# Kernel optimization log

Hardware: AMD Instinct MI355X
Metric: run time of the kernel (lower is better)

Reference implementation:

```python
import jax, jax.numpy as jnp
import numpy as np

N_HEADS = 16


def setup_inputs() -> dict:
    key = jax.random.key(0)
    ks = jax.random.split(key, 7)
    B, S, D = 2, 2048, 1024
    x = jax.random.normal(ks[0], (B, S, D), dtype=jnp.float32)
    attn_mask = jax.random.normal(ks[1], (S, S), dtype=jnp.float32) * 0.1
    attn_bias = jax.random.normal(ks[2], (B, S, S), dtype=jnp.float32) * 0.1
    Wqkv = jax.random.normal(ks[3], (D, 3 * D), dtype=jnp.float32) * (D ** -0.5)
    bqkv = jnp.zeros((3 * D,), dtype=jnp.float32)
    Wout = jax.random.normal(ks[4], (D, D), dtype=jnp.float32) * (D ** -0.5)
    bout = jnp.zeros((D,), dtype=jnp.float32)
    return {"x": x, "attn_mask": attn_mask, "attn_bias": attn_bias,
            "Wqkv": Wqkv, "bqkv": bqkv, "Wout": Wout, "bout": bout}


def reference(x, attn_mask, attn_bias, Wqkv, bqkv, Wout, bout):
    B, S, D = x.shape
    H = N_HEADS
    hd = D // H
    # qkv projection: [B,S,3D] -> [3,B,H,S,hd]
    qkv = (x @ Wqkv + bqkv).reshape(B, S, 3, H, hd).transpose(2, 0, 3, 1, 4)
    q, k, v = qkv[0], qkv[1], qkv[2]
    scores = jnp.einsum('bhqd,bhkd->bhqk', q, k) / (hd ** 0.5)
    scores = scores + attn_mask[None, None, :, :] + attn_bias[:, None, :, :]
    attn = jax.nn.softmax(scores, axis=-1)  # dropout p=0.0 (eval)
    out = jnp.einsum('bhqk,bhkd->bhqd', attn, v)
    out = out.transpose(0, 2, 1, 3).reshape(B, S, D)
    return out @ Wout + bout
```

## Files before the change

### kernel.cpp

```cpp
#include <hip/hip_runtime.h>
#include <hip/hip_bf16.h>


#define S_LEN 2048
#define DMODEL 1024
#define NH 16
#define HD 64

typedef __bf16 bf16x8 __attribute__((ext_vector_type(8)));
typedef __bf16 bf16x4 __attribute__((ext_vector_type(4)));
typedef __bf16 bf16x2v __attribute__((ext_vector_type(2)));
typedef float f32x4 __attribute__((ext_vector_type(4)));
typedef short s16x4 __attribute__((ext_vector_type(4)));

#define GLD_LDS16(g, l)                                              \
  __builtin_amdgcn_global_load_lds(                                  \
      (const __attribute__((address_space(1))) unsigned int*)(g),    \
      (__attribute__((address_space(3))) unsigned int*)(l), 16, 0, 0)

#if __has_builtin(__builtin_amdgcn_mfma_f32_16x16x16bf16_1k)
#define HAVE_MFMA_16x16x16_BF16 1
#else
#define HAVE_MFMA_16x16x16_BF16 0
#endif

#if __has_builtin(__builtin_amdgcn_exp2f)
#define EXP2F(x) __builtin_amdgcn_exp2f(x)
#else
static __device__ __forceinline__ float EXP2F(float x) {
  float r;
  asm volatile("v_exp_f32 %0, %1" : "=v"(r) : "v"(x));
  return r;
}
#endif

#define LOG2E 1.44269504f

__global__ __launch_bounds__(256) void preprocess(
    const float* __restrict__ x, const float* __restrict__ mask,
    const float* __restrict__ bias, const float* __restrict__ Wqkv,
    const float* __restrict__ Wout, __bf16* __restrict__ Xb,
    __bf16* __restrict__ Wt, __bf16* __restrict__ Wt2,
    __bf16* __restrict__ MB) {
  __shared__ __align__(16) char smem[64 * 65 * 4];
  const int bid = blockIdx.x;
  const int tid = threadIdx.x;

  if (bid < 4096) {
    int i = bid * 256 + tid;
    float4 v = ((const float4*)x)[i];
    bf16x4 o = {(__bf16)v.x, (__bf16)v.y, (__bf16)v.z, (__bf16)v.w};
    *(bf16x4*)&Xb[(size_t)i * 4] = o;
  } else if (bid < 5120) {
    const float* W;
    __bf16* Wo;
    int ncols, n0, k0;
    if (bid < 4864) {
      int id = bid - 4096;
      W = Wqkv; Wo = Wt; ncols = 3072;
      n0 = (id % 48) * 64; k0 = (id / 48) * 64;
    } else {
      int id = bid - 4864;
      W = Wout; Wo = Wt2; ncols = 1024;
      n0 = (id & 15) * 64; k0 = (id >> 4) * 64;
    }
    float(*tile)[65] = (float(*)[65])smem;
    {
      int c = tid & 63, r4 = tid >> 6;
#pragma unroll
      for (int p = 0; p < 16; ++p) {
        int r = r4 + p * 4;
        tile[r][c] = W[(size_t)(k0 + r) * ncols + n0 + c];
      }
    }
    __syncthreads();
    {
      int cc = (tid & 31) * 2, r8 = tid >> 5;
#pragma unroll
      for (int p = 0; p < 8; ++p) {
        int rr = r8 + p * 8;
        bf16x2v o = {(__bf16)tile[cc][rr], (__bf16)tile[cc + 1][rr]};
        *(bf16x2v*)&Wo[(size_t)(n0 + rr) * 1024 + k0 + cc] = o;
      }
    }
  } else {
    int id = bid - 5120;
    const int kt = id & 31, qt = (id >> 5) & 31, b = id >> 10;
    __bf16(*sm)[68] = (__bf16(*)[68])smem;
    {
      const int r0 = tid >> 4;
      const int cc = (tid & 15) * 4;
      const float* mrow = mask + (size_t)(qt * 64) * S_LEN + kt * 64;
      const float* brow =
          bias + ((size_t)b * S_LEN + qt * 64) * S_LEN + kt * 64;
#pragma unroll
      for (int p = 0; p < 4; ++p) {
        int r = r0 + p * 16;
        float4 m = *(const float4*)(mrow + (size_t)r * S_LEN + cc);
        float4 a = *(const float4*)(brow + (size_t)r * S_LEN + cc);
        sm[r][cc + 0] = (__bf16)((m.x + a.x) * LOG2E);
        sm[r][cc + 1] = (__bf16)((m.y + a.y) * LOG2E);
        sm[r][cc + 2] = (__bf16)((m.z + a.z) * LOG2E);
        sm[r][cc + 3] = (__bf16)((m.w + a.w) * LOG2E);
      }
    }
    __syncthreads();
    const int w = tid >> 6, lane = tid & 63;
    const int quad = lane >> 4, cl = lane & 15;
    __bf16 vals[16];
#pragma unroll
    for (int ct = 0; ct < 4; ++ct) {
      bf16x4 v = *(const bf16x4*)&sm[w * 16 + cl][ct * 16 + quad * 4];
      *(bf16x4*)&vals[ct * 4] = v;
    }
    __bf16* op =
        MB + (((size_t)(b * 32 + qt) * 32 + kt) * 4096) + (w * 64 + lane) * 16;
    *(bf16x8*)op = *(bf16x8*)&vals[0];
    *(bf16x8*)(op + 8) = *(bf16x8*)&vals[8];
  }
}

__global__ __launch_bounds__(256) void gemm_qkv_mfma(
    const __bf16* __restrict__ Xb, const __bf16* __restrict__ Wt,
    const float* __restrict__ bqkv, __bf16* __restrict__ Qb,
    __bf16* __restrict__ Kb, __bf16* __restrict__ Vtb) {
  __shared__ __align__(16) __bf16 As[128 * 32];
  __shared__ __align__(16) __bf16 Bs[128 * 32];
  const int tid = threadIdx.x;
  const int w = tid >> 6, lane = tid & 63;
  const int c = lane & 15, quad = lane >> 4;
  const int wm = w >> 1, wn = w & 1;
  const int rowBase = blockIdx.y * 128;
  const int colBase = blockIdx.x * 128;

  f32x4 acc[4][4] = {};

  const __bf16* gA0 =
      Xb + (size_t)(rowBase + w * 32 + (lane >> 2)) * 1024 + (lane & 3) * 8;
  const __bf16* gB0 =
      Wt + (size_t)(colBase + w * 32 + (lane >> 2)) * 1024 + (lane & 3) * 8;
  __bf16* lA0 = &As[(w * 32) * 32];
  __bf16* lB0 = &Bs[(w * 32) * 32];

  for (int k0 = 0; k0 < 1024; k0 += 32) {
    __syncthreads();
#pragma unroll
    for (int p = 0; p < 2; ++p) {
      GLD_LDS16(gA0 + (size_t)p * 16 * 1024 + k0, lA0 + p * 16 * 32);
      GLD_LDS16(gB0 + (size_t)p * 16 * 1024 + k0, lB0 + p * 16 * 32);
    }
    __syncthreads();

    bf16x8 af[4], bfr[4];
#pragma unroll
    for (int mt = 0; mt < 4; ++mt)
      af[mt] = *(const bf16x8*)&As[(wm * 64 + mt * 16 + c) * 32 + quad * 8];
#pragma unroll
    for (int nt = 0; nt < 4; ++nt)
      bfr[nt] = *(const bf16x8*)&Bs[(wn * 64 + nt * 16 + c) * 32 + quad * 8];
#pragma unroll
    for (int mt = 0; mt < 4; ++mt)
#pragma unroll
      for (int nt = 0; nt < 4; ++nt)
        acc[mt][nt] = __builtin_amdgcn_mfma_f32_16x16x32_bf16(
            af[mt], bfr[nt], acc[mt][nt], 0, 0, 0);
  }

#pragma unroll
  for (int mt = 0; mt < 4; ++mt) {
    int row0 = rowBase + wm * 64 + mt * 16 + quad * 4;
#pragma unroll
    for (int nt = 0; nt < 4; ++nt) {
      int col = colBase + wn * 64 + nt * 16 + c;
      float bias = bqkv[col];
      int three = col >> 10;
      int h = (col & 1023) >> 6;
      int d = col & 63;
#pragma unroll
      for (int r = 0; r < 4; ++r) {
        int rr = row0 + r;
        int bb = rr >> 11, s = rr & 2047;
        float val = acc[mt][nt][r] + bias;
        size_t ho = (size_t)(bb * NH + h);
        if (three == 0)
          Qb[(ho * S_LEN + s) * HD + d] = (__bf16)val;
        else if (three == 1)
          Kb[(ho * S_LEN + s) * HD + d] = (__bf16)val;
        else
          Vtb[(ho * HD + d) * S_LEN + s] = (__bf16)val;
      }
    }
  }
}

__global__ __launch_bounds__(256) void attn_mfma(
    const __bf16* __restrict__ Qb, const __bf16* __restrict__ Kb,
    const __bf16* __restrict__ Vtb, const __bf16* __restrict__ MB,
    __bf16* __restrict__ PO, float* __restrict__ L) {
  const int qt = blockIdx.x, h = blockIdx.y;
  const int b = blockIdx.z >> 1, half = blockIdx.z & 1;
  const int kt0 = half * 16;
  const int tid = threadIdx.x;
  const int w = tid >> 6;
  const int lane = tid & 63;
  const int c = lane & 15;
  const int quad = lane >> 4;

  __shared__ __align__(16) __bf16 Ks[2][64 * 64];
  __shared__ __align__(16) __bf16 Vs[2][64 * 64];
#if !HAVE_MFMA_16x16x16_BF16
  __shared__ __align__(16) __bf16 P2[4][16 * 72];
#endif

  const size_t headoff = (size_t)(b * NH + h) * S_LEN * HD;
  const __bf16* Qg = Qb + headoff + (size_t)(qt * 128) * HD;
  const __bf16* Kg = Kb + headoff;
  const __bf16* Vg = Vtb + headoff;
  const __bf16* MBq0 = MB + ((size_t)(b * 32 + qt * 2 + 0) * 32 + kt0) * 4096 +
                       (w * 64 + lane) * 16;
  const __bf16* MBq1 = MB + ((size_t)(b * 32 + qt * 2 + 1) * 32 + kt0) * 4096 +
                       (w * 64 + lane) * 16;

  __bf16* POx = PO + (size_t)half * 4194304;
  float* Lx = L + half * 65536;

  const int f0 = tid >> 3, f1 = f0 + 32;
  const int j = tid & 7;
  const int sj0 = j ^ (f0 & 7);
  const int sj1 = j ^ (f1 & 7);
  const int lds0 = tid * 8;
  const int lds1 = (256 + tid) * 8;

  bf16x8 qa[2][2];
#pragma unroll
  for (int g = 0; g < 2; ++g) {
    qa[g][0] = *(const bf16x8*)(Qg + (g * 64 + w * 16 + c) * HD + quad * 8);
    qa[g][1] =
        *(const bf16x8*)(Qg + (g * 64 + w * 16 + c) * HD + quad * 8 + 32);
  }

  const int rs0 = (quad ^ (c & 7)) * 8;
  const int rs1 = ((quad + 4) ^ (c & 7)) * 8;

  f32x4 Oa[2][4] = {};
  f32x4 psum[2] = {};

  const int kb0 = kt0 * 64;
  GLD_LDS16(Kg + (size_t)(kb0 + f0) * HD + sj0 * 8, &Ks[0][lds0]);
  GLD_LDS16(Kg + (size_t)(kb0 + f1) * HD + sj1 * 8, &Ks[0][lds1]);
  GLD_LDS16(Vg + (size_t)f0 * S_LEN + kb0 + sj0 * 8, &Vs[0][lds0]);
  GLD_LDS16(Vg + (size_t)f1 * S_LEN + kb0 + sj1 * 8, &Vs[0][lds1]);

  const __bf16* kgp0 = Kg + (size_t)(kb0 + 64 + f0) * HD + sj0 * 8;
  const __bf16* kgp1 = Kg + (size_t)(kb0 + 64 + f1) * HD + sj1 * 8;
  const __bf16* vgp0 = Vg + (size_t)f0 * S_LEN + kb0 + 64 + sj0 * 8;
  const __bf16* vgp1 = Vg + (size_t)f1 * S_LEN + kb0 + 64 + sj1 * 8;

  bf16x8 rMB[2][2];
  rMB[0][0] = *(const bf16x8*)MBq0;
  rMB[0][1] = *(const bf16x8*)(MBq0 + 8);
  rMB[1][0] = *(const bf16x8*)MBq1;
  rMB[1][1] = *(const bf16x8*)(MBq1 + 8);

  __syncthreads();

  const float c1 = 0.125f * LOG2E;

#pragma unroll 2
  for (int lkt = 0; lkt < 16; ++lkt) {
    const int cur = lkt & 1, nxt = cur ^ 1;
    bf16x8 nMB[2][2];
    {
      const __bf16* m0 = MBq0 + (size_t)(lkt + 1) * 4096;
      const __bf16* m1 = MBq1 + (size_t)(lkt + 1) * 4096;
      nMB[0][0] = *(const bf16x8*)m0;
      nMB[0][1] = *(const bf16x8*)(m0 + 8);
      nMB[1][0] = *(const bf16x8*)m1;
      nMB[1][1] = *(const bf16x8*)(m1 + 8);
    }
    if (lkt < 15) {
      GLD_LDS16(kgp0, &Ks[nxt][lds0]);
      GLD_LDS16(kgp1, &Ks[nxt][lds1]);
      GLD_LDS16(vgp0, &Vs[nxt][lds0]);
      GLD_LDS16(vgp1, &Vs[nxt][lds1]);
    }
    kgp0 += 64 * HD;
    kgp1 += 64 * HD;
    vgp0 += 64;
    vgp1 += 64;

    bf16x8 kf0[4], kf1[4];
#pragma unroll
    for (int ct = 0; ct < 4; ++ct) {
      kf0[ct] = *(const bf16x8*)&Ks[cur][(ct * 16 + c) * 64 + rs0];
      kf1[ct] = *(const bf16x8*)&Ks[cur][(ct * 16 + c) * 64 + rs1];
    }

    f32x4 sv[2][4];
    __builtin_amdgcn_s_setprio(1);
#pragma unroll
    for (int g = 0; g < 2; ++g)
#pragma unroll
      for (int ct = 0; ct < 4; ++ct) {
        f32x4 a = {};
        a = __builtin_amdgcn_mfma_f32_16x16x32_bf16(kf0[ct], qa[g][0], a, 0,
                                                    0, 0);
        a = __builtin_amdgcn_mfma_f32_16x16x32_bf16(kf1[ct], qa[g][1], a, 0,
                                                    0, 0);
        sv[g][ct] = a;
      }
    __builtin_amdgcn_s_setprio(0);

#if HAVE_MFMA_16x16x16_BF16
    s16x4 vf[4][4];
#pragma unroll
    for (int ft = 0; ft < 4; ++ft) {
      const int fr = ft * 16 + c;
#pragma unroll
      for (int ct = 0; ct < 4; ++ct) {
        const int chunk = ((ct * 2 + (quad >> 1)) ^ (fr & 7)) * 8 +
                          (quad & 1) * 4;
        vf[ft][ct] = *(const s16x4*)&Vs[cur][fr * 64 + chunk];
      }
    }
#endif

    s16x4 pb[2][4];
#pragma unroll
    for (int g = 0; g < 2; ++g)
#pragma unroll
      for (int ct = 0; ct < 4; ++ct) {
        f32x4 pv;
#pragma unroll
        for (int r = 0; r < 4; ++r) {
          float mb = (ct < 2) ? (float)rMB[g][0][ct * 4 + r]
                              : (float)rMB[g][1][(ct - 2) * 4 + r];
          pv[r] = EXP2F(sv[g][ct][r] * c1 + mb);
        }
        psum[g] += pv;
        __bf16 t4[4];
#pragma unroll
        for (int r = 0; r < 4; ++r) t4[r] = (__bf16)pv[r];
        pb[g][ct] = *(s16x4*)t4;
      }
#pragma unroll
    for (int g = 0; g < 2; ++g) {
      rMB[g][0] = nMB[g][0];
      rMB[g][1] = nMB[g][1];
    }

#if HAVE_MFMA_16x16x16_BF16
    __builtin_amdgcn_s_setprio(1);
#pragma unroll
    for (int g = 0; g < 2; ++g)
#pragma unroll
      for (int ft = 0; ft < 4; ++ft)
#pragma unroll
        for (int ct = 0; ct < 4; ++ct)
          Oa[g][ft] = __builtin_amdgcn_mfma_f32_16x16x16bf16_1k(
              vf[ft][ct], pb[g][ct], Oa[g][ft], 0, 0, 0);
    __builtin_amdgcn_s_setprio(0);
#else
#pragma unroll
    for (int g = 0; g < 2; ++g) {
#pragma unroll
      for (int ct = 0; ct < 4; ++ct)
        *(bf16x4*)&P2[w][c * 72 + ct * 16 + quad * 4] = *(bf16x4*)&pb[g][ct];
      bf16x8 pf0 = *(const bf16x8*)&P2[w][c * 72 + quad * 8];
      bf16x8 pf1 = *(const bf16x8*)&P2[w][c * 72 + 32 + quad * 8];
#pragma unroll
      for (int ft = 0; ft < 4; ++ft) {
        const int fr = ft * 16 + c;
        bf16x8 vf0 = *(const bf16x8*)&Vs[cur][fr * 64 + rs0];
        bf16x8 vf1 = *(const bf16x8*)&Vs[cur][fr * 64 + rs1];
        Oa[g][ft] = __builtin_amdgcn_mfma_f32_16x16x32_bf16(vf0, pf0,
                                                            Oa[g][ft], 0, 0, 0);
        Oa[g][ft] = __builtin_amdgcn_mfma_f32_16x16x32_bf16(vf1, pf1,
                                                            Oa[g][ft], 0, 0, 0);
      }
    }
#endif

    __syncthreads();
  }
#pragma unroll
  for (int g = 0; g < 2; ++g) {
    float lsum = psum[g][0] + psum[g][1] + psum[g][2] + psum[g][3];
    lsum += __shfl_xor(lsum, 16);
    lsum += __shfl_xor(lsum, 32);
    if (lane < 16)
      Lx[(size_t)(b * NH + h) * S_LEN + qt * 128 + g * 64 + w * 16 + c] = lsum;
    __bf16* orow = POx +
                   (size_t)(b * S_LEN + qt * 128 + g * 64 + w * 16 + c) *
                       DMODEL +
                   h * HD;
#pragma unroll
    for (int ft = 0; ft < 4; ++ft) {
      __bf16 t4[4];
#pragma unroll
      for (int r = 0; r < 4; ++r) t4[r] = (__bf16)Oa[g][ft][r];
      *(bf16x4*)(orow + ft * 16 + quad * 4) = *(bf16x4*)t4;
    }
  }
}

__global__ __launch_bounds__(256) void combine(const __bf16* __restrict__ PO,
                                               const float* __restrict__ L,
                                               __bf16* __restrict__ AOb) {
  const int i = blockIdx.x * 256 + threadIdx.x;
  const size_t e = (size_t)i * 8;
  const int hidx = (int)(e >> 6) & 15;
  const int s = (int)(e >> 10) & 2047;
  const int b = (int)(e >> 21);
  const size_t li = ((size_t)(b * NH + hidx) << 11) + s;
  const float invl = 1.0f / (L[li] + L[65536 + li]);
  bf16x8 a = *(const bf16x8*)&PO[e];
  bf16x8 c = *(const bf16x8*)&PO[4194304 + e];
  __bf16 o[8];
#pragma unroll
  for (int k = 0; k < 8; ++k)
    o[k] = (__bf16)(((float)a[k] + (float)c[k]) * invl);
  *(bf16x8*)&AOb[e] = *(bf16x8*)o;
}

__global__ __launch_bounds__(256) void gemm_out_mfma(
    const __bf16* __restrict__ AOb, const __bf16* __restrict__ Wt2,
    const float* __restrict__ bout, float* __restrict__ Out) {
  __shared__ __align__(16) __bf16 As[128 * 32];
  __shared__ __align__(16) __bf16 Bs[64 * 32];
  const int tid = threadIdx.x;
  const int w = tid >> 6, lane = tid & 63;
  const int c = lane & 15, quad = lane >> 4;
  const int rowBase = blockIdx.y * 128;
  const int colBase = blockIdx.x * 64;

  f32x4 acc[2][4] = {};

  const __bf16* gA0 =
      AOb + (size_t)(rowBase + w * 32 + (lane >> 2)) * 1024 + (lane & 3) * 8;
  const __bf16* gB0 =
      Wt2 + (size_t)(colBase + w * 16 + (lane >> 2)) * 1024 + (lane & 3) * 8;
  __bf16* lA0 = &As[(w * 32) * 32];
  __bf16* lB0 = &Bs[(w * 16) * 32];

  for (int k0 = 0; k0 < 1024; k0 += 32) {
    __syncthreads();
#pragma unroll
    for (int p = 0; p < 2; ++p)
      GLD_LDS16(gA0 + (size_t)p * 16 * 1024 + k0, lA0 + p * 16 * 32);
    GLD_LDS16(gB0 + k0, lB0);
    __syncthreads();

    bf16x8 af[2], bfr[4];
#pragma unroll
    for (int mt = 0; mt < 2; ++mt)
      af[mt] = *(const bf16x8*)&As[(w * 32 + mt * 16 + c) * 32 + quad * 8];
#pragma unroll
    for (int nt = 0; nt < 4; ++nt)
      bfr[nt] = *(const bf16x8*)&Bs[(nt * 16 + c) * 32 + quad * 8];
#pragma unroll
    for (int mt = 0; mt < 2; ++mt)
#pragma unroll
      for (int nt = 0; nt < 4; ++nt)
        acc[mt][nt] = __builtin_amdgcn_mfma_f32_16x16x32_bf16(
            af[mt], bfr[nt], acc[mt][nt], 0, 0, 0);
  }

#pragma unroll
  for (int mt = 0; mt < 2; ++mt) {
    int row0 = rowBase + w * 32 + mt * 16 + quad * 4;
#pragma unroll
    for (int nt = 0; nt < 4; ++nt) {
      int col = colBase + nt * 16 + c;
      float bias = bout[col];
#pragma unroll
      for (int r = 0; r < 4; ++r)
        Out[(size_t)(row0 + r) * 1024 + col] = acc[mt][nt][r] + bias;
    }
  }
}

extern "C" void kernel_launch(void* const* d_in, const int* in_sizes, int n_in,
                              void* d_out, int out_size, void* d_ws,
                              size_t ws_size, hipStream_t stream) {
  const float* x = (const float*)d_in[0];
  const float* attn_mask = (const float*)d_in[1];
  const float* attn_bias = (const float*)d_in[2];
  const float* Wqkv = (const float*)d_in[3];
  const float* bqkv = (const float*)d_in[4];
  const float* Wout = (const float*)d_in[5];
  const float* bout = (const float*)d_in[6];
  float* out = (float*)d_out;

  __bf16* base = (__bf16*)d_ws;
  __bf16* Xb = base;
  __bf16* PO = base;
  __bf16* Wt = base + 4194304;
  __bf16* Qb = base + 8388608;
  __bf16* Kb = base + 12582912;
  __bf16* Vtb = base + 16777216;
  __bf16* AOb = base + 16777216;
  __bf16* MB = base + 20971520;
  __bf16* Wt2 = base + 29360128;
  float* Lf = (float*)d_out;

  preprocess<<<7168, 256, 0, stream>>>(x, attn_mask, attn_bias, Wqkv, Wout,
                                       Xb, Wt, Wt2, MB);
  gemm_qkv_mfma<<<dim3(24, 32), 256, 0, stream>>>(Xb, Wt, bqkv, Qb, Kb, Vtb);
  attn_mfma<<<dim3(16, NH, 4), 256, 0, stream>>>(Qb, Kb, Vtb, MB, PO, Lf);
  combine<<<2048, 256, 0, stream>>>(PO, Lf, AOb);
  gemm_out_mfma<<<dim3(16, 32), 256, 0, stream>>>(AOb, Wt2, bout, out);
}
```

Baseline: 278.4 us.

## Reuse mask across batches, coalesce V transpose via LDS, restructure attention loop

The preprocess mask+bias block now loads the mask tile once and loops over both batches, cutting mask reads and the grid size. The QKV GEMM epilogue stages V tiles through shared memory so the transposed Vt writes become 16-byte coalesced stores instead of scattered 2-byte ones. The attention kernel interleaves QK MFMA and exp per row group, loads mask-bias tiles just in time instead of prefetching them, and gains a launch-bounds occupancy hint of 3 blocks. Together these aim to reduce memory traffic and register pressure, at the cost of extra syncs and possibly exposed load latency.

```diff
diff --git a/kernel.cpp b/kernel.cpp
--- a/kernel.cpp
+++ b/kernel.cpp
@@ -85,38 +85,42 @@
     }
   } else {
     int id = bid - 5120;
-    const int kt = id & 31, qt = (id >> 5) & 31, b = id >> 10;
+    const int kt = id & 31, qt = id >> 5;
     __bf16(*sm)[68] = (__bf16(*)[68])smem;
-    {
-      const int r0 = tid >> 4;
-      const int cc = (tid & 15) * 4;
-      const float* mrow = mask + (size_t)(qt * 64) * S_LEN + kt * 64;
+    const int r0 = tid >> 4;
+    const int cc = (tid & 15) * 4;
+    const float* mrow = mask + (size_t)(qt * 64) * S_LEN + kt * 64;
+    float4 mld[4];
+#pragma unroll
+    for (int p = 0; p < 4; ++p)
+      mld[p] = *(const float4*)(mrow + (size_t)(r0 + p * 16) * S_LEN + cc);
+    const int w = tid >> 6, lane = tid & 63;
+    const int quad = lane >> 4, cl = lane & 15;
+    for (int b = 0; b < 2; ++b) {
       const float* brow =
           bias + ((size_t)b * S_LEN + qt * 64) * S_LEN + kt * 64;
 #pragma unroll
       for (int p = 0; p < 4; ++p) {
         int r = r0 + p * 16;
-        float4 m = *(const float4*)(mrow + (size_t)r * S_LEN + cc);
         float4 a = *(const float4*)(brow + (size_t)r * S_LEN + cc);
-        sm[r][cc + 0] = (__bf16)((m.x + a.x) * LOG2E);
-        sm[r][cc + 1] = (__bf16)((m.y + a.y) * LOG2E);
-        sm[r][cc + 2] = (__bf16)((m.z + a.z) * LOG2E);
-        sm[r][cc + 3] = (__bf16)((m.w + a.w) * LOG2E);
-      }
-    }
-    __syncthreads();
-    const int w = tid >> 6, lane = tid & 63;
-    const int quad = lane >> 4, cl = lane & 15;
-    __bf16 vals[16];
-#pragma unroll
-    for (int ct = 0; ct < 4; ++ct) {
-      bf16x4 v = *(const bf16x4*)&sm[w * 16 + cl][ct * 16 + quad * 4];
-      *(bf16x4*)&vals[ct * 4] = v;
-    }
-    __bf16* op =
-        MB + (((size_t)(b * 32 + qt) * 32 + kt) * 4096) + (w * 64 + lane) * 16;
-    *(bf16x8*)op = *(bf16x8*)&vals[0];
-    *(bf16x8*)(op + 8) = *(bf16x8*)&vals[8];
+        sm[r][cc + 0] = (__bf16)((mld[p].x + a.x) * LOG2E);
+        sm[r][cc + 1] = (__bf16)((mld[p].y + a.y) * LOG2E);
+        sm[r][cc + 2] = (__bf16)((mld[p].z + a.z) * LOG2E);
+        sm[r][cc + 3] = (__bf16)((mld[p].w + a.w) * LOG2E);
+      }
+      __syncthreads();
+      __bf16 vals[16];
+#pragma unroll
+      for (int ct = 0; ct < 4; ++ct) {
+        bf16x4 v = *(const bf16x4*)&sm[w * 16 + cl][ct * 16 + quad * 4];
+        *(bf16x4*)&vals[ct * 4] = v;
+      }
+      __bf16* op = MB + (((size_t)(b * 32 + qt) * 32 + kt) * 4096) +
+                   (w * 64 + lane) * 16;
+      *(bf16x8*)op = *(bf16x8*)&vals[0];
+      *(bf16x8*)(op + 8) = *(bf16x8*)&vals[8];
+      __syncthreads();
+    }
   }
 }
 
@@ -124,8 +128,9 @@
     const __bf16* __restrict__ Xb, const __bf16* __restrict__ Wt,
     const float* __restrict__ bqkv, __bf16* __restrict__ Qb,
     __bf16* __restrict__ Kb, __bf16* __restrict__ Vtb) {
-  __shared__ __align__(16) __bf16 As[128 * 32];
-  __shared__ __align__(16) __bf16 Bs[128 * 32];
+  __shared__ __align__(16) __bf16 shm[4 * 64 * 72];
+  __bf16* As = shm;
+  __bf16* Bs = shm + 4096;
   const int tid = threadIdx.x;
   const int w = tid >> 6, lane = tid & 63;
   const int c = lane & 15, quad = lane >> 4;
@@ -166,40 +171,69 @@
             af[mt], bfr[nt], acc[mt][nt], 0, 0, 0);
   }
 
-#pragma unroll
-  for (int mt = 0; mt < 4; ++mt) {
-    int row0 = rowBase + wm * 64 + mt * 16 + quad * 4;
+  if (colBase < 2048) {
+#pragma unroll
+    for (int mt = 0; mt < 4; ++mt) {
+      int row0 = rowBase + wm * 64 + mt * 16 + quad * 4;
+#pragma unroll
+      for (int nt = 0; nt < 4; ++nt) {
+        int col = colBase + wn * 64 + nt * 16 + c;
+        float bias = bqkv[col];
+        int three = col >> 10;
+        int h = (col & 1023) >> 6;
+        int d = col & 63;
+#pragma unroll
+        for (int r = 0; r < 4; ++r) {
+          int rr = row0 + r;
+          int bb = rr >> 11, s = rr & 2047;
+          float val = acc[mt][nt][r] + bias;
+          size_t ho = (size_t)(bb * NH + h);
+          if (three == 0)
+            Qb[(ho * S_LEN + s) * HD + d] = (__bf16)val;
+          else
+            Kb[(ho * S_LEN + s) * HD + d] = (__bf16)val;
+        }
+      }
+    }
+  } else {
+    __syncthreads();
+    __bf16* Tt = shm + w * (64 * 72);
+    const int cols0 = colBase + wn * 64;
+    const int rows0 = rowBase + wm * 64;
+    const int hq = (cols0 & 1023) >> 6;
+    const int bb = rows0 >> 11;
+    const int sBase = rows0 & 2047;
 #pragma unroll
     for (int nt = 0; nt < 4; ++nt) {
-      int col = colBase + wn * 64 + nt * 16 + c;
-      float bias = bqkv[col];
-      int three = col >> 10;
-      int h = (col & 1023) >> 6;
-      int d = col & 63;
-#pragma unroll
-      for (int r = 0; r < 4; ++r) {
-        int rr = row0 + r;
-        int bb = rr >> 11, s = rr & 2047;
-        float val = acc[mt][nt][r] + bias;
-        size_t ho = (size_t)(bb * NH + h);
-        if (three == 0)
-          Qb[(ho * S_LEN + s) * HD + d] = (__bf16)val;
-        else if (three == 1)
-          Kb[(ho * S_LEN + s) * HD + d] = (__bf16)val;
-        else
-          Vtb[(ho * HD + d) * S_LEN + s] = (__bf16)val;
-      }
-    }
-  }
-}
-
-__global__ __launch_bounds__(256) void attn_mfma(
+      float bias = bqkv[cols0 + nt * 16 + c];
+#pragma unroll
+      for (int mt = 0; mt < 4; ++mt) {
+        __bf16 t4[4];
+#pragma unroll
+        for (int r = 0; r < 4; ++r) t4[r] = (__bf16)(acc[mt][nt][r] + bias);
+        *(bf16x4*)&Tt[(nt * 16 + c) * 72 + mt * 16 + quad * 4] =
+            *(bf16x4*)t4;
+      }
+    }
+    __syncthreads();
+    const size_t vbase = ((size_t)(bb * NH + hq) * HD) * S_LEN;
+    const int s0 = (lane & 7) * 8;
+    const int dl0 = lane >> 3;
+#pragma unroll
+    for (int dt = 0; dt < 8; ++dt) {
+      int dl = dt * 8 + dl0;
+      bf16x8 v = *(const bf16x8*)&Tt[dl * 72 + s0];
+      *(bf16x8*)&Vtb[vbase + (size_t)dl * S_LEN + sBase + s0] = v;
+    }
+  }
+}
+
+__global__ __launch_bounds__(256, 3) void attn_mfma(
     const __bf16* __restrict__ Qb, const __bf16* __restrict__ Kb,
     const __bf16* __restrict__ Vtb, const __bf16* __restrict__ MB,
     __bf16* __restrict__ PO, float* __restrict__ L) {
   const int qt = blockIdx.x, h = blockIdx.y;
   const int b = blockIdx.z >> 1, half = blockIdx.z & 1;
-  const int kt0 = half * 16;
   const int tid = threadIdx.x;
   const int w = tid >> 6;
   const int lane = tid & 63;
@@ -213,12 +247,15 @@
 #endif
 
   const size_t headoff = (size_t)(b * NH + h) * S_LEN * HD;
+  const int kv0 = half * 1024;
   const __bf16* Qg = Qb + headoff + (size_t)(qt * 128) * HD;
-  const __bf16* Kg = Kb + headoff;
+  const __bf16* Kg = Kb + headoff + (size_t)kv0 * HD;
   const __bf16* Vg = Vtb + headoff;
-  const __bf16* MBq0 = MB + ((size_t)(b * 32 + qt * 2 + 0) * 32 + kt0) * 4096 +
+  const __bf16* mbp0 = MB +
+                       ((size_t)(b * 32 + qt * 2 + 0) * 32 + half * 16) * 4096 +
                        (w * 64 + lane) * 16;
-  const __bf16* MBq1 = MB + ((size_t)(b * 32 + qt * 2 + 1) * 32 + kt0) * 4096 +
+  const __bf16* mbp1 = MB +
+                       ((size_t)(b * 32 + qt * 2 + 1) * 32 + half * 16) * 4096 +
                        (w * 64 + lane) * 16;
 
   __bf16* POx = PO + (size_t)half * 4194304;
@@ -245,40 +282,32 @@
   f32x4 Oa[2][4] = {};
   f32x4 psum[2] = {};
 
-  const int kb0 = kt0 * 64;
-  GLD_LDS16(Kg + (size_t)(kb0 + f0) * HD + sj0 * 8, &Ks[0][lds0]);
-  GLD_LDS16(Kg + (size_t)(kb0 + f1) * HD + sj1 * 8, &Ks[0][lds1]);
-  GLD_LDS16(Vg + (size_t)f0 * S_LEN + kb0 + sj0 * 8, &Vs[0][lds0]);
-  GLD_LDS16(Vg + (size_t)f1 * S_LEN + kb0 + sj1 * 8, &Vs[0][lds1]);
-
-  const __bf16* kgp0 = Kg + (size_t)(kb0 + 64 + f0) * HD + sj0 * 8;
-  const __bf16* kgp1 = Kg + (size_t)(kb0 + 64 + f1) * HD + sj1 * 8;
-  const __bf16* vgp0 = Vg + (size_t)f0 * S_LEN + kb0 + 64 + sj0 * 8;
-  const __bf16* vgp1 = Vg + (size_t)f1 * S_LEN + kb0 + 64 + sj1 * 8;
+  GLD_LDS16(Kg + (size_t)f0 * HD + sj0 * 8, &Ks[0][lds0]);
+  GLD_LDS16(Kg + (size_t)f1 * HD + sj1 * 8, &Ks[0][lds1]);
+  GLD_LDS16(Vg + (size_t)f0 * S_LEN + kv0 + sj0 * 8, &Vs[0][lds0]);
+  GLD_LDS16(Vg + (size_t)f1 * S_LEN + kv0 + sj1 * 8, &Vs[0][lds1]);
+
+  const __bf16* kgp0 = Kg + (size_t)(64 + f0) * HD + sj0 * 8;
+  const __bf16* kgp1 = Kg + (size_t)(64 + f1) * HD + sj1 * 8;
+  const __bf16* vgp0 = Vg + (size_t)f0 * S_LEN + kv0 + 64 + sj0 * 8;
+  const __bf16* vgp1 = Vg + (size_t)f1 * S_LEN + kv0 + 64 + sj1 * 8;
 
   bf16x8 rMB[2][2];
-  rMB[0][0] = *(const bf16x8*)MBq0;
-  rMB[0][1] = *(const bf16x8*)(MBq0 + 8);
-  rMB[1][0] = *(const bf16x8*)MBq1;
-  rMB[1][1] = *(const bf16x8*)(MBq1 + 8);
+  rMB[0][0] = *(const bf16x8*)mbp0;
+  rMB[0][1] = *(const bf16x8*)(mbp0 + 8);
+  rMB[1][0] = *(const bf16x8*)mbp1;
+  rMB[1][1] = *(const bf16x8*)(mbp1 + 8);
+  mbp0 += 4096;
+  mbp1 += 4096;
 
   __syncthreads();
 
   const float c1 = 0.125f * LOG2E;
 
 #pragma unroll 2
-  for (int lkt = 0; lkt < 16; ++lkt) {
-    const int cur = lkt & 1, nxt = cur ^ 1;
-    bf16x8 nMB[2][2];
-    {
-      const __bf16* m0 = MBq0 + (size_t)(lkt + 1) * 4096;
-      const __bf16* m1 = MBq1 + (size_t)(lkt + 1) * 4096;
-      nMB[0][0] = *(const bf16x8*)m0;
-      nMB[0][1] = *(const bf16x8*)(m0 + 8);
-      nMB[1][0] = *(const bf16x8*)m1;
-      nMB[1][1] = *(const bf16x8*)(m1 + 8);
-    }
-    if (lkt < 15) {
+  for (int t = 0; t < 16; ++t) {
+    const int cur = t & 1, nxt = cur ^ 1;
+    if (t < 15) {
       GLD_LDS16(kgp0, &Ks[nxt][lds0]);
       GLD_LDS16(kgp1, &Ks[nxt][lds1]);
       GLD_LDS16(vgp0, &Vs[nxt][lds0]);
@@ -296,10 +325,11 @@
       kf1[ct] = *(const bf16x8*)&Ks[cur][(ct * 16 + c) * 64 + rs1];
     }
 
-    f32x4 sv[2][4];
-    __builtin_amdgcn_s_setprio(1);
-#pragma unroll
-    for (int g = 0; g < 2; ++g)
+    s16x4 pb[2][4];
+#pragma unroll
+    for (int g = 0; g < 2; ++g) {
+      f32x4 sv[4];
+      __builtin_amdgcn_s_setprio(1);
 #pragma unroll
       for (int ct = 0; ct < 4; ++ct) {
         f32x4 a = {};
@@ -307,9 +337,30 @@
                                                     0, 0);
         a = __builtin_amdgcn_mfma_f32_16x16x32_bf16(kf1[ct], qa[g][1], a, 0,
                                                     0, 0);
-        sv[g][ct] = a;
-      }
-    __builtin_amdgcn_s_setprio(0);
+        sv[ct] = a;
+      }
+      __builtin_amdgcn_s_setprio(0);
+#pragma unroll
+      for (int ct = 0; ct < 4; ++ct) {
+        f32x4 pv;
+#pragma unroll
+        for (int r = 0; r < 4; ++r) {
+          float mb = (ct < 2) ? (float)rMB[g][0][ct * 4 + r]
+                              : (float)rMB[g][1][(ct - 2) * 4 + r];
+          pv[r] = EXP2F(sv[ct][r] * c1 + mb);
+        }
+        psum[g] += pv;
+        __bf16 t4[4];
+#pragma unroll
+        for (int r = 0; r < 4; ++r) t4[r] = (__bf16)pv[r];
+        pb[g][ct] = *(s16x4*)t4;
+      }
+      const __bf16* mp = g ? mbp1 : mbp0;
+      rMB[g][0] = *(const bf16x8*)mp;
+      rMB[g][1] = *(const bf16x8*)(mp + 8);
+    }
+    mbp0 += 4096;
+    mbp1 += 4096;
 
 #if HAVE_MFMA_16x16x16_BF16
     s16x4 vf[4][4];
@@ -323,33 +374,6 @@
         vf[ft][ct] = *(const s16x4*)&Vs[cur][fr * 64 + chunk];
       }
     }
-#endif
-
-    s16x4 pb[2][4];
-#pragma unroll
-    for (int g = 0; g < 2; ++g)
-#pragma unroll
-      for (int ct = 0; ct < 4; ++ct) {
-        f32x4 pv;
-#pragma unroll
-        for (int r = 0; r < 4; ++r) {
-          float mb = (ct < 2) ? (float)rMB[g][0][ct * 4 + r]
-                              : (float)rMB[g][1][(ct - 2) * 4 + r];
-          pv[r] = EXP2F(sv[g][ct][r] * c1 + mb);
-        }
-        psum[g] += pv;
-        __bf16 t4[4];
-#pragma unroll
-        for (int r = 0; r < 4; ++r) t4[r] = (__bf16)pv[r];
-        pb[g][ct] = *(s16x4*)t4;
-      }
-#pragma unroll
-    for (int g = 0; g < 2; ++g) {
-      rMB[g][0] = nMB[g][0];
-      rMB[g][1] = nMB[g][1];
-    }
-
-#if HAVE_MFMA_16x16x16_BF16
     __builtin_amdgcn_s_setprio(1);
 #pragma unroll
     for (int g = 0; g < 2; ++g)
@@ -371,11 +395,11 @@
 #pragma unroll
       for (int ft = 0; ft < 4; ++ft) {
         const int fr = ft * 16 + c;
-        bf16x8 vf0 = *(const bf16x8*)&Vs[cur][fr * 64 + rs0];
-        bf16x8 vf1 = *(const bf16x8*)&Vs[cur][fr * 64 + rs1];
-        Oa[g][ft] = __builtin_amdgcn_mfma_f32_16x16x32_bf16(vf0, pf0,
+        bf16x8 vv0 = *(const bf16x8*)&Vs[cur][fr * 64 + rs0];
+        bf16x8 vv1 = *(const bf16x8*)&Vs[cur][fr * 64 + rs1];
+        Oa[g][ft] = __builtin_amdgcn_mfma_f32_16x16x32_bf16(vv0, pf0,
                                                             Oa[g][ft], 0, 0, 0);
-        Oa[g][ft] = __builtin_amdgcn_mfma_f32_16x16x32_bf16(vf1, pf1,
+        Oa[g][ft] = __builtin_amdgcn_mfma_f32_16x16x32_bf16(vv1, pf1,
                                                             Oa[g][ft], 0, 0, 0);
       }
     }
@@ -383,6 +407,7 @@
 
     __syncthreads();
   }
+
 #pragma unroll
   for (int g = 0; g < 2; ++g) {
     float lsum = psum[g][0] + psum[g][1] + psum[g][2] + psum[g][3];
@@ -504,7 +529,7 @@
   __bf16* Wt2 = base + 29360128;
   float* Lf = (float*)d_out;
 
-  preprocess<<<7168, 256, 0, stream>>>(x, attn_mask, attn_bias, Wqkv, Wout,
+  preprocess<<<6144, 256, 0, stream>>>(x, attn_mask, attn_bias, Wqkv, Wout,
                                        Xb, Wt, Wt2, MB);
   gemm_qkv_mfma<<<dim3(24, 32), 256, 0, stream>>>(Xb, Wt, bqkv, Qb, Kb, Vtb);
   attn_mfma<<<dim3(16, NH, 4), 256, 0, stream>>>(Qb, Kb, Vtb, MB, PO, Lf);
```

Result: faster. 263.2 us (-5.5%).
